# Kernel optimization log

Hardware: AMD Instinct MI355X
Metric: run time of the kernel (lower is better)

The kernel has to match this reference:

```python
import jax, jax.numpy as jnp
import numpy as np

N = 100_000   # nodes
E = 1_600_000 # edges (avg degree 16)
D = 128       # feature dim (input = hidden = output = mlp hidden)
L = 3         # GIN layers
EPS = 0.0     # init_eps, not learned


def setup_inputs() -> dict:
    key = jax.random.key(0)
    ks = jax.random.split(key, 7)
    feat = jax.random.normal(ks[0], (N, D), jnp.float32)
    # scale weights ~ 1/sqrt(fan_in) for numerically sane activations
    W1 = jax.random.normal(ks[1], (L, D, D), jnp.float32) / np.float32(np.sqrt(D))
    b1 = jax.random.normal(ks[2], (L, D), jnp.float32) * 0.01
    W2 = jax.random.normal(ks[3], (L, D, D), jnp.float32) / np.float32(np.sqrt(D))
    b2 = jax.random.normal(ks[4], (L, D), jnp.float32) * 0.01
    src = jax.random.randint(ks[5], (E,), 0, N, dtype=jnp.int32)
    dst = jax.random.randint(ks[6], (E,), 0, N, dtype=jnp.int32)
    return {"feat": feat, "W1": W1, "b1": b1, "W2": W2, "b2": b2,
            "src": src, "dst": dst}


def reference(feat, W1, b1, W2, b2, src, dst):
    h = feat
    for i in range(L):
        # sum-aggregate neighbor (source) features into destination nodes
        neigh = jax.ops.segment_sum(h[src], dst, num_segments=N)  # [N, D]
        rst = (1.0 + EPS) * h + neigh
        # 2-layer MLP: hidden layer uses act+norm(none), last layer is plain linear
        if i < L - 1:
            h1 = jax.nn.relu(rst @ W1[i] + b1[i])
            h2 = h1 @ W2[i] + b2[i]
            h = jax.nn.relu(h2)  # ApplyNodeFunc: norm(none) -> relu
        else:
            # last GIN layer: activation 'none' everywhere
            h1 = rst @ W1[i] + b1[i]
            h = h1 @ W2[i] + b2[i]
    return h
```

## Files before the change

### kernel.cpp

```cpp
#include <hip/hip_runtime.h>
#include <hip/hip_bf16.h>

#define D 128
#define NBUCK_SHIFT 9

typedef __bf16 bf16x8 __attribute__((ext_vector_type(8)));
typedef float f32x4 __attribute__((ext_vector_type(4)));
typedef unsigned int u32x4 __attribute__((ext_vector_type(4)));
typedef unsigned short u16x4_t __attribute__((ext_vector_type(4)));
typedef unsigned short u16x8_t __attribute__((ext_vector_type(8)));

__device__ __forceinline__ float b2f(unsigned short u) {
    unsigned int x = ((unsigned int)u) << 16;
    return __builtin_bit_cast(float, x);
}
__device__ __forceinline__ unsigned short f2b(float f) {
    __hip_bfloat16 h = __float2bfloat16(f);
    return __builtin_bit_cast(unsigned short, h);
}

__device__ __forceinline__ void acc8(float* acc, u32x4 x) {
#pragma unroll
    for (int r = 0; r < 4; ++r) {
        acc[2 * r]     += __builtin_bit_cast(float, x[r] << 16);
        acc[2 * r + 1] += __builtin_bit_cast(float, x[r] & 0xffff0000u);
    }
}

__global__ __launch_bounds__(256) void coarse_hist_kernel(
        const int* __restrict__ dst, int* __restrict__ bco, int E, int nbuck) {
    __shared__ int s[256];
    int t = threadIdx.x;
    s[t] = 0;
    __syncthreads();
    for (int i = blockIdx.x * 256 + t; i < E; i += gridDim.x * 256)
        atomicAdd(&s[dst[i] >> NBUCK_SHIFT], 1);
    __syncthreads();
    if (t < nbuck && s[t] > 0) atomicAdd(&bco[t], s[t]);
}

__global__ __launch_bounds__(256) void bucket_scan_kernel(
        const int* __restrict__ bco, int* __restrict__ bbase, int nbuck, int E) {
    __shared__ int s[256];
    int t = threadIdx.x;
    int c = (t < nbuck) ? bco[t] : 0;
    s[t] = c;
    __syncthreads();
    for (int o = 1; o < 256; o <<= 1) {
        int y = (t >= o) ? s[t - o] : 0;
        __syncthreads();
        s[t] += y;
        __syncthreads();
    }
    if (t < nbuck) bbase[t] = s[t] - c;
    if (t == 0) bbase[nbuck] = E;
}

__global__ __launch_bounds__(256) void bucket_kernel(
        const int* __restrict__ src, const int* __restrict__ dst,
        const int* __restrict__ bbase, int* __restrict__ bcursor,
        int2* __restrict__ pairs, int E, int nbuck) {
    __shared__ int lcnt[256];
    __shared__ int lbase[256];
    int t = threadIdx.x;
    int base = blockIdx.x * 4096;
    if (t < nbuck) lcnt[t] = 0;
    __syncthreads();
    int d[16], s[16];
#pragma unroll
    for (int k = 0; k < 16; ++k) {
        int i = base + t + k * 256;
        if (i < E) {
            d[k] = dst[i];
            s[k] = src[i];
            atomicAdd(&lcnt[d[k] >> NBUCK_SHIFT], 1);
        } else {
            d[k] = -1;
            s[k] = 0;
        }
    }
    __syncthreads();
    if (t < nbuck) {
        int c = lcnt[t];
        int g = (c > 0) ? atomicAdd(&bcursor[t], c) : 0;
        lbase[t] = bbase[t] + g;
        lcnt[t] = 0;
    }
    __syncthreads();
#pragma unroll
    for (int k = 0; k < 16; ++k) {
        if (d[k] >= 0) {
            int b = d[k] >> NBUCK_SHIFT;
            int r = atomicAdd(&lcnt[b], 1);
            pairs[lbase[b] + r] = make_int2(s[k], d[k]);
        }
    }
}

__global__ __launch_bounds__(1024) void bucket_build_kernel(
        const int2* __restrict__ pairs, const int* __restrict__ bbase,
        int* __restrict__ row_ptr, int* __restrict__ col, int N, int E) {
    __shared__ int cnt[512];
    __shared__ int off[512];
    int t = threadIdx.x;
    int b = blockIdx.x;
    int s0 = bbase[b], s1 = bbase[b + 1];
    if (t < 512) cnt[t] = 0;
    __syncthreads();
    for (int i = s0 + t; i < s1; i += 1024)
        atomicAdd(&cnt[pairs[i].y & 511], 1);
    __syncthreads();
    int c = (t < 512) ? cnt[t] : 0;
    if (t < 512) off[t] = c;
    __syncthreads();
    for (int o = 1; o < 512; o <<= 1) {
        int y = (t < 512 && t >= o) ? off[t - o] : 0;
        __syncthreads();
        if (t < 512) off[t] += y;
        __syncthreads();
    }
    int v0 = b << NBUCK_SHIFT;
    if (t < 512) {
        int ex = off[t] - c;
        off[t] = ex;
        cnt[t] = 0;
        if (v0 + t < N) row_ptr[v0 + t] = s0 + ex;
    }
    __syncthreads();
    for (int i = s0 + t; i < s1; i += 1024) {
        int2 p = pairs[i];
        int li = p.y & 511;
        int slot = s0 + off[li] + atomicAdd(&cnt[li], 1);
        col[slot] = p.x;
    }
    if (b == 0 && t == 0) row_ptr[N] = E;
}

__global__ void f32_to_bf16_kernel(const float4* __restrict__ in, ushort4* __restrict__ out, int n4) {
    int i = blockIdx.x * blockDim.x + threadIdx.x;
    if (i < n4) {
        float4 f = in[i];
        ushort4 o;
        o.x = f2b(f.x); o.y = f2b(f.y); o.z = f2b(f.z); o.w = f2b(f.w);
        out[i] = o;
    }
}

__global__ void wtrans_kernel(const float* __restrict__ W1, const float* __restrict__ W2,
                              unsigned short* __restrict__ W1L, unsigned short* __restrict__ W2L,
                              int total) {
    int i = blockIdx.x * blockDim.x + threadIdx.x;
    if (i < total) {
        int l = i >> 14;
        int rem = i & 16383;
        int k = rem >> 7;
        int n = rem & 127;
        int nt = n >> 4, l15 = n & 15;
        int kb = k >> 5, lg = (k >> 3) & 3, j = k & 7;
        int o = ((l * 32 + nt * 4 + kb) * 64 + lg * 16 + l15) * 8 + j;
        W1L[o] = f2b(W1[i]);
        W2L[o] = f2b(W2[i]);
    }
}

__global__ __launch_bounds__(256) void agg_kernel(
        const unsigned short* __restrict__ h, const int* __restrict__ row_ptr,
        const int* __restrict__ col, unsigned short* __restrict__ rst, int N) {
    int lane = threadIdx.x & 63;
    int i = lane & 15;
    int j = lane >> 4;
    int v = blockIdx.x * 4 + (threadIdx.x >> 6);
    if (v >= N) return;

    const unsigned short* hb = h + i * 8;
    int e0 = row_ptr[v], e1 = row_ptr[v + 1];

    float accA[8], accB[8], accC[8], accD[8];
#pragma unroll
    for (int r = 0; r < 8; ++r) { accA[r] = 0.f; accB[r] = 0.f; accC[r] = 0.f; accD[r] = 0.f; }

    if (j == 0) {
        u32x4 x = *(const u32x4*)(hb + (size_t)v * D);
        acc8(accA, x);
    }

    int e = e0 + j;
    for (; e + 12 < e1; e += 16) {
        int u0 = col[e];
        int u1 = col[e + 4];
        int u2 = col[e + 8];
        int u3 = col[e + 12];
        u32x4 x0 = *(const u32x4*)(hb + (size_t)u0 * D);
        u32x4 x1 = *(const u32x4*)(hb + (size_t)u1 * D);
        u32x4 x2 = *(const u32x4*)(hb + (size_t)u2 * D);
        u32x4 x3 = *(const u32x4*)(hb + (size_t)u3 * D);
        acc8(accA, x0);
        acc8(accB, x1);
        acc8(accC, x2);
        acc8(accD, x3);
    }
    for (; e + 4 < e1; e += 8) {
        int u0 = col[e];
        int u1 = col[e + 4];
        u32x4 x0 = *(const u32x4*)(hb + (size_t)u0 * D);
        u32x4 x1 = *(const u32x4*)(hb + (size_t)u1 * D);
        acc8(accA, x0);
        acc8(accB, x1);
    }
    if (e < e1) {
        u32x4 x0 = *(const u32x4*)(hb + (size_t)col[e] * D);
        acc8(accA, x0);
    }

    unsigned short outv[8];
#pragma unroll
    for (int r = 0; r < 8; ++r) {
        float s = (accA[r] + accB[r]) + (accC[r] + accD[r]);
        s += __shfl_xor(s, 16);
        s += __shfl_xor(s, 32);
        outv[r] = f2b(s);
    }
    if (j == 0) {
        u16x8_t o;
#pragma unroll
        for (int r = 0; r < 8; ++r) o[r] = outv[r];
        *(u16x8_t*)(rst + (size_t)v * D + i * 8) = o;
    }
}

__global__ __launch_bounds__(256, 4) void mlp_kernel(
        const unsigned short* __restrict__ A, const unsigned short* __restrict__ W1L,
        const unsigned short* __restrict__ W2L, const float* __restrict__ b1,
        const float* __restrict__ b2, unsigned short* __restrict__ hOut,
        float* __restrict__ fOut, int mode, int ntiles, int N) {
    __shared__ float b1s[128], b2s[128];
    __shared__ unsigned short tilebuf[4 * 2560];
    int tid = threadIdx.x;
    if (tid < 128) b1s[tid] = b1[tid];
    else b2s[tid - 128] = b2[tid - 128];
    __syncthreads();
    int wave = tid >> 6, lane = tid & 63, l15 = lane & 15, lg = lane >> 4;
    unsigned short* buf = tilebuf + wave * 2560;
    int tile = blockIdx.x * 4 + wave;
    if (tile >= ntiles) return;
    int v0 = tile << 4;

    bf16x8 bfrag[4];
    const unsigned short* arow = A + (size_t)(v0 + l15) * D + lg * 8;
#pragma unroll
    for (int kb = 0; kb < 4; ++kb) bfrag[kb] = *(const bf16x8*)(arow + kb * 32);

    f32x4 acc[8];
#pragma unroll
    for (int nt = 0; nt < 8; ++nt) acc[nt] = (f32x4){0.f, 0.f, 0.f, 0.f};
#pragma unroll
    for (int kb = 0; kb < 4; ++kb)
#pragma unroll
        for (int nt = 0; nt < 8; ++nt) {
            bf16x8 wf = *(const bf16x8*)(W1L + ((nt * 4 + kb) * 64 + lane) * 8);
            acc[nt] = __builtin_amdgcn_mfma_f32_16x16x32_bf16(wf, bfrag[kb], acc[nt], 0, 0, 0);
        }
#pragma unroll
    for (int nt = 0; nt < 8; ++nt) {
        f32x4 bias = *(const f32x4*)(b1s + nt * 16 + lg * 4);
        int kb2 = nt >> 1;
        int lgk = (nt & 1) * 2 + (lg >> 1);
        int U = kb2 * 80 + l15 * 5 + lgk;
        u16x4_t o;
#pragma unroll
        for (int r = 0; r < 4; ++r) {
            float x = acc[nt][r] + bias[r];
            if (mode == 0) x = fmaxf(x, 0.f);
            o[r] = f2b(x);
        }
        *(u16x4_t*)(buf + U * 8 + (lg & 1) * 4) = o;
    }
    bf16x8 bf2[4];
#pragma unroll
    for (int kb = 0; kb < 4; ++kb)
        bf2[kb] = *(const bf16x8*)(buf + (kb * 80 + l15 * 5 + lg) * 8);
#pragma unroll
    for (int nt = 0; nt < 8; ++nt) acc[nt] = (f32x4){0.f, 0.f, 0.f, 0.f};
#pragma unroll
    for (int kb = 0; kb < 4; ++kb)
#pragma unroll
        for (int nt = 0; nt < 8; ++nt) {
            bf16x8 wf = *(const bf16x8*)(W2L + ((nt * 4 + kb) * 64 + lane) * 8);
            acc[nt] = __builtin_amdgcn_mfma_f32_16x16x32_bf16(wf, bf2[kb], acc[nt], 0, 0, 0);
        }
    int m = v0 + l15;
    if (m < N) {
#pragma unroll
        for (int nt = 0; nt < 8; ++nt) {
            f32x4 bias = *(const f32x4*)(b2s + nt * 16 + lg * 4);
            int c0 = nt * 16 + lg * 4;
            if (mode == 0) {
                u16x4_t o;
#pragma unroll
                for (int r = 0; r < 4; ++r) o[r] = f2b(fmaxf(acc[nt][r] + bias[r], 0.f));
                *(u16x4_t*)(hOut + (size_t)m * D + c0) = o;
            } else {
                f32x4 o;
#pragma unroll
                for (int r = 0; r < 4; ++r) o[r] = acc[nt][r] + bias[r];
                *(f32x4*)(fOut + (size_t)m * D + c0) = o;
            }
        }
    }
}

extern "C" void kernel_launch(void* const* d_in, const int* in_sizes, int n_in,
                              void* d_out, int out_size, void* d_ws, size_t ws_size,
                              hipStream_t stream) {
    const float* feat = (const float*)d_in[0];
    const float* W1 = (const float*)d_in[1];
    const float* b1 = (const float*)d_in[2];
    const float* W2 = (const float*)d_in[3];
    const float* b2 = (const float*)d_in[4];
    const int* src = (const int*)d_in[5];
    const int* dst = (const int*)d_in[6];

    const int N = in_sizes[0] / D;
    const int L = in_sizes[2] / D;
    const int E = in_sizes[5];

    char* w = (char*)d_ws;
    size_t off = 0;
    auto alloc = [&](size_t bytes) {
        void* p = w + off;
        off = (off + bytes + 255) & ~(size_t)255;
        return p;
    };
    unsigned short* bufA = (unsigned short*)alloc((size_t)N * D * 2);
    unsigned short* bufB = (unsigned short*)alloc((size_t)N * D * 2);
    size_t unionBytes = (size_t)N * D * 2;
    if ((size_t)E * 8 > unionBytes) unionBytes = (size_t)E * 8;
    unsigned short* bufR = (unsigned short*)alloc(unionBytes);
    int2* pairs = (int2*)bufR;
    int* col = (int*)alloc((size_t)E * 4);
    int* row_ptr = (int*)alloc((size_t)(N + 1) * 4);
    int* bco = (int*)alloc(512 * 4);
    int* bcursor = bco + 256;
    int* bbase = (int*)alloc(257 * 4);
    unsigned short* W1L = (unsigned short*)alloc((size_t)L * 16384 * 2);
    unsigned short* W2L = (unsigned short*)alloc((size_t)L * 16384 * 2);

    int nbuck = (N + (1 << NBUCK_SHIFT) - 1) >> NBUCK_SHIFT;

    hipMemsetAsync(bco, 0, 512 * 4, stream);
    coarse_hist_kernel<<<512, 256, 0, stream>>>(dst, bco, E, nbuck);
    bucket_scan_kernel<<<1, 256, 0, stream>>>(bco, bbase, nbuck, E);
    bucket_kernel<<<(E + 4095) / 4096, 256, 0, stream>>>(src, dst, bbase, bcursor, pairs, E, nbuck);
    bucket_build_kernel<<<nbuck, 1024, 0, stream>>>(pairs, bbase, row_ptr, col, N, E);

    int n4 = N * D / 4;
    f32_to_bf16_kernel<<<(n4 + 255) / 256, 256, 0, stream>>>((const float4*)feat, (ushort4*)bufA, n4);
    int wtotal = L * D * D;
    wtrans_kernel<<<(wtotal + 255) / 256, 256, 0, stream>>>(W1, W2, W1L, W2L, wtotal);

    int ntiles = (N + 15) / 16;
    int aggBlocks = (N + 3) / 4;
    int mlpGrid = (ntiles + 3) / 4;
    const unsigned short* hin[3] = {bufA, bufB, bufA};
    unsigned short* hout[3] = {bufB, bufA, nullptr};
    for (int i = 0; i < L; ++i) {
        int mode = (i == L - 1) ? 1 : 0;
        agg_kernel<<<aggBlocks, 256, 0, stream>>>(hin[i], row_ptr, col, bufR, N);
        mlp_kernel<<<mlpGrid, 256, 0, stream>>>(bufR, W1L + (size_t)i * 16384, W2L + (size_t)i * 16384,
                                                b1 + i * D, b2 + i * D, hout[i], (float*)d_out,
                                                mode, ntiles, N);
    }
}
```

Baseline: 447.9 us.

## Process two nodes per wave in aggregation and trim CSR build overheads

Measured after the change: 471.8 us. 5.3% more time.

```diff
diff --git a/kernel.cpp b/kernel.cpp
--- a/kernel.cpp
+++ b/kernel.cpp
@@ -3,32 +3,32 @@
 
 #define D 128
 #define NBUCK_SHIFT 9
+#define CH_BLOCKS 128
 
 typedef __bf16 bf16x8 __attribute__((ext_vector_type(8)));
 typedef float f32x4 __attribute__((ext_vector_type(4)));
+typedef float f32x2 __attribute__((ext_vector_type(2)));
 typedef unsigned int u32x4 __attribute__((ext_vector_type(4)));
 typedef unsigned short u16x4_t __attribute__((ext_vector_type(4)));
 typedef unsigned short u16x8_t __attribute__((ext_vector_type(8)));
 
-__device__ __forceinline__ float b2f(unsigned short u) {
-    unsigned int x = ((unsigned int)u) << 16;
-    return __builtin_bit_cast(float, x);
-}
 __device__ __forceinline__ unsigned short f2b(float f) {
     __hip_bfloat16 h = __float2bfloat16(f);
     return __builtin_bit_cast(unsigned short, h);
 }
 
-__device__ __forceinline__ void acc8(float* acc, u32x4 x) {
+__device__ __forceinline__ void acc4x2(f32x2* acc, u32x4 x) {
 #pragma unroll
     for (int r = 0; r < 4; ++r) {
-        acc[2 * r]     += __builtin_bit_cast(float, x[r] << 16);
-        acc[2 * r + 1] += __builtin_bit_cast(float, x[r] & 0xffff0000u);
+        f32x2 v;
+        v[0] = __builtin_bit_cast(float, x[r] << 16);
+        v[1] = __builtin_bit_cast(float, x[r] & 0xffff0000u);
+        acc[r] += v;
     }
 }
 
 __global__ __launch_bounds__(256) void coarse_hist_kernel(
-        const int* __restrict__ dst, int* __restrict__ bco, int E, int nbuck) {
+        const int* __restrict__ dst, int* __restrict__ bcoP, int E) {
     __shared__ int s[256];
     int t = threadIdx.x;
     s[t] = 0;
@@ -36,14 +36,16 @@
     for (int i = blockIdx.x * 256 + t; i < E; i += gridDim.x * 256)
         atomicAdd(&s[dst[i] >> NBUCK_SHIFT], 1);
     __syncthreads();
-    if (t < nbuck && s[t] > 0) atomicAdd(&bco[t], s[t]);
+    bcoP[blockIdx.x * 256 + t] = s[t];
 }
 
 __global__ __launch_bounds__(256) void bucket_scan_kernel(
-        const int* __restrict__ bco, int* __restrict__ bbase, int nbuck, int E) {
+        const int* __restrict__ bcoP, int* __restrict__ bbase, int* __restrict__ bcursor,
+        int nblk, int nbuck, int E) {
     __shared__ int s[256];
     int t = threadIdx.x;
-    int c = (t < nbuck) ? bco[t] : 0;
+    int c = 0;
+    for (int b = 0; b < nblk; ++b) c += bcoP[b * 256 + t];
     s[t] = c;
     __syncthreads();
     for (int o = 1; o < 256; o <<= 1) {
@@ -52,14 +54,15 @@
         s[t] += y;
         __syncthreads();
     }
-    if (t < nbuck) bbase[t] = s[t] - c;
+    bbase[t] = s[t] - c;
+    bcursor[t] = 0;
     if (t == 0) bbase[nbuck] = E;
 }
 
 __global__ __launch_bounds__(256) void bucket_kernel(
         const int* __restrict__ src, const int* __restrict__ dst,
         const int* __restrict__ bbase, int* __restrict__ bcursor,
-        int2* __restrict__ pairs, int E, int nbuck) {
+        unsigned int* __restrict__ pairs, int E, int nbuck) {
     __shared__ int lcnt[256];
     __shared__ int lbase[256];
     int t = threadIdx.x;
@@ -92,13 +95,13 @@
         if (d[k] >= 0) {
             int b = d[k] >> NBUCK_SHIFT;
             int r = atomicAdd(&lcnt[b], 1);
-            pairs[lbase[b] + r] = make_int2(s[k], d[k]);
+            pairs[lbase[b] + r] = ((unsigned)s[k] << NBUCK_SHIFT) | (unsigned)(d[k] & 511);
         }
     }
 }
 
 __global__ __launch_bounds__(1024) void bucket_build_kernel(
-        const int2* __restrict__ pairs, const int* __restrict__ bbase,
+        const unsigned int* __restrict__ pairs, const int* __restrict__ bbase,
         int* __restrict__ row_ptr, int* __restrict__ col, int N, int E) {
     __shared__ int cnt[512];
     __shared__ int off[512];
@@ -108,7 +111,7 @@
     if (t < 512) cnt[t] = 0;
     __syncthreads();
     for (int i = s0 + t; i < s1; i += 1024)
-        atomicAdd(&cnt[pairs[i].y & 511], 1);
+        atomicAdd(&cnt[pairs[i] & 511], 1);
     __syncthreads();
     int c = (t < 512) ? cnt[t] : 0;
     if (t < 512) off[t] = c;
@@ -128,29 +131,26 @@
     }
     __syncthreads();
     for (int i = s0 + t; i < s1; i += 1024) {
-        int2 p = pairs[i];
-        int li = p.y & 511;
+        unsigned int p = pairs[i];
+        int li = p & 511;
         int slot = s0 + off[li] + atomicAdd(&cnt[li], 1);
-        col[slot] = p.x;
+        col[slot] = (int)(p >> NBUCK_SHIFT);
     }
     if (b == 0 && t == 0) row_ptr[N] = E;
 }
 
-__global__ void f32_to_bf16_kernel(const float4* __restrict__ in, ushort4* __restrict__ out, int n4) {
+__global__ void prep_kernel(const float4* __restrict__ feat4, ushort4* __restrict__ h4, int n4,
+                            const float* __restrict__ W1, const float* __restrict__ W2,
+                            unsigned short* __restrict__ W1L, unsigned short* __restrict__ W2L,
+                            int wtotal) {
     int i = blockIdx.x * blockDim.x + threadIdx.x;
     if (i < n4) {
-        float4 f = in[i];
+        float4 f = feat4[i];
         ushort4 o;
         o.x = f2b(f.x); o.y = f2b(f.y); o.z = f2b(f.z); o.w = f2b(f.w);
-        out[i] = o;
-    }
-}
-
-__global__ void wtrans_kernel(const float* __restrict__ W1, const float* __restrict__ W2,
-                              unsigned short* __restrict__ W1L, unsigned short* __restrict__ W2L,
-                              int total) {
-    int i = blockIdx.x * blockDim.x + threadIdx.x;
-    if (i < total) {
+        h4[i] = o;
+    }
+    if (i < wtotal) {
         int l = i >> 14;
         int rem = i & 16383;
         int k = rem >> 7;
@@ -163,68 +163,94 @@
     }
 }
 
-__global__ __launch_bounds__(256) void agg_kernel(
+__global__ __launch_bounds__(256, 4) void agg_kernel(
         const unsigned short* __restrict__ h, const int* __restrict__ row_ptr,
         const int* __restrict__ col, unsigned short* __restrict__ rst, int N) {
     int lane = threadIdx.x & 63;
     int i = lane & 15;
     int j = lane >> 4;
-    int v = blockIdx.x * 4 + (threadIdx.x >> 6);
-    if (v >= N) return;
-
+    int w = blockIdx.x * 4 + (threadIdx.x >> 6);
+    int vA = w * 2;
+    if (vA >= N) return;
+    int vB = vA + 1;
+    bool hasB = vB < N;
     const unsigned short* hb = h + i * 8;
-    int e0 = row_ptr[v], e1 = row_ptr[v + 1];
-
-    float accA[8], accB[8], accC[8], accD[8];
-#pragma unroll
-    for (int r = 0; r < 8; ++r) { accA[r] = 0.f; accB[r] = 0.f; accC[r] = 0.f; accD[r] = 0.f; }
+
+    int e0A = row_ptr[vA], e1A = row_ptr[vA + 1];
+    int e1B = hasB ? row_ptr[vB + 1] : 0;
+    int e0B = hasB ? e1A : 0;
+
+    f32x2 aA0[4], aA1[4], aB0[4], aB1[4];
+#pragma unroll
+    for (int r = 0; r < 4; ++r) {
+        aA0[r] = (f32x2){0.f, 0.f}; aA1[r] = (f32x2){0.f, 0.f};
+        aB0[r] = (f32x2){0.f, 0.f}; aB1[r] = (f32x2){0.f, 0.f};
+    }
 
     if (j == 0) {
-        u32x4 x = *(const u32x4*)(hb + (size_t)v * D);
-        acc8(accA, x);
-    }
-
-    int e = e0 + j;
-    for (; e + 12 < e1; e += 16) {
-        int u0 = col[e];
-        int u1 = col[e + 4];
-        int u2 = col[e + 8];
-        int u3 = col[e + 12];
-        u32x4 x0 = *(const u32x4*)(hb + (size_t)u0 * D);
-        u32x4 x1 = *(const u32x4*)(hb + (size_t)u1 * D);
-        u32x4 x2 = *(const u32x4*)(hb + (size_t)u2 * D);
-        u32x4 x3 = *(const u32x4*)(hb + (size_t)u3 * D);
-        acc8(accA, x0);
-        acc8(accB, x1);
-        acc8(accC, x2);
-        acc8(accD, x3);
-    }
-    for (; e + 4 < e1; e += 8) {
-        int u0 = col[e];
-        int u1 = col[e + 4];
-        u32x4 x0 = *(const u32x4*)(hb + (size_t)u0 * D);
-        u32x4 x1 = *(const u32x4*)(hb + (size_t)u1 * D);
-        acc8(accA, x0);
-        acc8(accB, x1);
-    }
-    if (e < e1) {
-        u32x4 x0 = *(const u32x4*)(hb + (size_t)col[e] * D);
-        acc8(accA, x0);
-    }
+        acc4x2(aA0, *(const u32x4*)(hb + (size_t)vA * D));
+        if (hasB) acc4x2(aB0, *(const u32x4*)(hb + (size_t)vB * D));
+    }
+
+    int eA = e0A + j, eB = e0B + j;
+    while (eA + 4 < e1A && eB + 4 < e1B) {
+        int a0 = col[eA], a1 = col[eA + 4];
+        int b0 = col[eB], b1 = col[eB + 4];
+        u32x4 xa0 = *(const u32x4*)(hb + (size_t)a0 * D);
+        u32x4 xa1 = *(const u32x4*)(hb + (size_t)a1 * D);
+        u32x4 xb0 = *(const u32x4*)(hb + (size_t)b0 * D);
+        u32x4 xb1 = *(const u32x4*)(hb + (size_t)b1 * D);
+        acc4x2(aA0, xa0); acc4x2(aA1, xa1);
+        acc4x2(aB0, xb0); acc4x2(aB1, xb1);
+        eA += 8; eB += 8;
+    }
+    while (eA + 4 < e1A) {
+        int a0 = col[eA], a1 = col[eA + 4];
+        u32x4 xa0 = *(const u32x4*)(hb + (size_t)a0 * D);
+        u32x4 xa1 = *(const u32x4*)(hb + (size_t)a1 * D);
+        acc4x2(aA0, xa0); acc4x2(aA1, xa1);
+        eA += 8;
+    }
+    if (eA < e1A) acc4x2(aA0, *(const u32x4*)(hb + (size_t)col[eA] * D));
+    while (eB + 4 < e1B) {
+        int b0 = col[eB], b1 = col[eB + 4];
+        u32x4 xb0 = *(const u32x4*)(hb + (size_t)b0 * D);
+        u32x4 xb1 = *(const u32x4*)(hb + (size_t)b1 * D);
+        acc4x2(aB0, xb0); acc4x2(aB1, xb1);
+        eB += 8;
+    }
+    if (eB < e1B) acc4x2(aB0, *(const u32x4*)(hb + (size_t)col[eB] * D));
 
     unsigned short outv[8];
 #pragma unroll
-    for (int r = 0; r < 8; ++r) {
-        float s = (accA[r] + accB[r]) + (accC[r] + accD[r]);
-        s += __shfl_xor(s, 16);
-        s += __shfl_xor(s, 32);
-        outv[r] = f2b(s);
+    for (int r = 0; r < 4; ++r) {
+        float s0 = aA0[r][0] + aA1[r][0];
+        float s1 = aA0[r][1] + aA1[r][1];
+        s0 += __shfl_xor(s0, 16); s0 += __shfl_xor(s0, 32);
+        s1 += __shfl_xor(s1, 16); s1 += __shfl_xor(s1, 32);
+        outv[2 * r] = f2b(s0);
+        outv[2 * r + 1] = f2b(s1);
     }
     if (j == 0) {
         u16x8_t o;
 #pragma unroll
         for (int r = 0; r < 8; ++r) o[r] = outv[r];
-        *(u16x8_t*)(rst + (size_t)v * D + i * 8) = o;
+        *(u16x8_t*)(rst + (size_t)vA * D + i * 8) = o;
+    }
+#pragma unroll
+    for (int r = 0; r < 4; ++r) {
+        float s0 = aB0[r][0] + aB1[r][0];
+        float s1 = aB0[r][1] + aB1[r][1];
+        s0 += __shfl_xor(s0, 16); s0 += __shfl_xor(s0, 32);
+        s1 += __shfl_xor(s1, 16); s1 += __shfl_xor(s1, 32);
+        outv[2 * r] = f2b(s0);
+        outv[2 * r + 1] = f2b(s1);
+    }
+    if (hasB && j == 0) {
+        u16x8_t o;
+#pragma unroll
+        for (int r = 0; r < 8; ++r) o[r] = outv[r];
+        *(u16x8_t*)(rst + (size_t)vB * D + i * 8) = o;
     }
 }
 
@@ -334,32 +360,33 @@
     unsigned short* bufA = (unsigned short*)alloc((size_t)N * D * 2);
     unsigned short* bufB = (unsigned short*)alloc((size_t)N * D * 2);
     size_t unionBytes = (size_t)N * D * 2;
-    if ((size_t)E * 8 > unionBytes) unionBytes = (size_t)E * 8;
+    if ((size_t)E * 4 > unionBytes) unionBytes = (size_t)E * 4;
     unsigned short* bufR = (unsigned short*)alloc(unionBytes);
-    int2* pairs = (int2*)bufR;
+    unsigned int* pairs = (unsigned int*)bufR;
     int* col = (int*)alloc((size_t)E * 4);
     int* row_ptr = (int*)alloc((size_t)(N + 1) * 4);
-    int* bco = (int*)alloc(512 * 4);
-    int* bcursor = bco + 256;
-    int* bbase = (int*)alloc(257 * 4);
+    int* bcoP = (int*)alloc((size_t)CH_BLOCKS * 256 * 4);
+    int* bbase = (int*)alloc(260 * 4);
+    int* bcursor = (int*)alloc(256 * 4);
     unsigned short* W1L = (unsigned short*)alloc((size_t)L * 16384 * 2);
     unsigned short* W2L = (unsigned short*)alloc((size_t)L * 16384 * 2);
 
     int nbuck = (N + (1 << NBUCK_SHIFT) - 1) >> NBUCK_SHIFT;
 
-    hipMemsetAsync(bco, 0, 512 * 4, stream);
-    coarse_hist_kernel<<<512, 256, 0, stream>>>(dst, bco, E, nbuck);
-    bucket_scan_kernel<<<1, 256, 0, stream>>>(bco, bbase, nbuck, E);
+    coarse_hist_kernel<<<CH_BLOCKS, 256, 0, stream>>>(dst, bcoP, E);
+    bucket_scan_kernel<<<1, 256, 0, stream>>>(bcoP, bbase, bcursor, CH_BLOCKS, nbuck, E);
     bucket_kernel<<<(E + 4095) / 4096, 256, 0, stream>>>(src, dst, bbase, bcursor, pairs, E, nbuck);
     bucket_build_kernel<<<nbuck, 1024, 0, stream>>>(pairs, bbase, row_ptr, col, N, E);
 
     int n4 = N * D / 4;
-    f32_to_bf16_kernel<<<(n4 + 255) / 256, 256, 0, stream>>>((const float4*)feat, (ushort4*)bufA, n4);
     int wtotal = L * D * D;
-    wtrans_kernel<<<(wtotal + 255) / 256, 256, 0, stream>>>(W1, W2, W1L, W2L, wtotal);
+    int prepGrid = (n4 > wtotal ? n4 : wtotal);
+    prep_kernel<<<(prepGrid + 255) / 256, 256, 0, stream>>>(
+        (const float4*)feat, (ushort4*)bufA, n4, W1, W2, W1L, W2L, wtotal);
 
     int ntiles = (N + 15) / 16;
-    int aggBlocks = (N + 3) / 4;
+    int nwaves = (N + 1) / 2;
+    int aggBlocks = (nwaves + 3) / 4;
     int mlpGrid = (ntiles + 3) / 4;
     const unsigned short* hin[3] = {bufA, bufB, bufA};
     unsigned short* hout[3] = {bufB, bufA, nullptr};
```
